# Kernel tuning notes

Measured on AMD Instinct MI355X. Metric: run time of the kernel, lower is better.

The kernel has to match this reference:

```python
import jax, jax.numpy as jnp
import numpy as np

NUM_HEADS = 16

def setup_inputs() -> dict:
    key = jax.random.key(0)
    ks = jax.random.split(key, 7)
    B, Q, K, D = 4, 512, 4096, 1024
    return {
        'query':  jax.random.normal(ks[0], (B, Q, D), dtype=jnp.float32),
        'memory': jax.random.normal(ks[1], (B, K, D), dtype=jnp.float32),
        'bias':   jax.random.normal(ks[2], (B, K), dtype=jnp.float32),
        'Wq': jax.random.normal(ks[3], (D, D), dtype=jnp.float32) * (D ** -0.5),
        'Wk': jax.random.normal(ks[4], (D, D), dtype=jnp.float32) * (D ** -0.5),
        'Wv': jax.random.normal(ks[5], (D, D), dtype=jnp.float32) * (D ** -0.5),
        'Wo': jax.random.normal(ks[6], (D, D), dtype=jnp.float32) * (D ** -0.5),
    }

def reference(query, memory, bias, Wq, Wk, Wv, Wo):
    B, Qn, _ = query.shape
    _, Kn, _ = memory.shape
    H = NUM_HEADS
    E = Wq.shape[1]
    dh = E // H
    scale = dh ** -0.5
    # projections (bias-free linears), split heads: [B, H, len, dh]
    q = (query @ Wq).reshape(B, Qn, H, dh).transpose(0, 2, 1, 3)
    k = (memory @ Wk).reshape(B, Kn, H, dh).transpose(0, 2, 1, 3)
    v = (memory @ Wv).reshape(B, Kn, H, dh).transpose(0, 2, 1, 3)
    scores = jnp.einsum('bhqd,bhkd->bhqk', q, k) * scale
    scores = scores + bias[:, None, None, :]          # additive support bias over K
    weights = jax.nn.softmax(scores, axis=-1)          # dropout p=0.0 -> identity
    out = jnp.einsum('bhqk,bhkd->bhqd', weights, v)
    out = out.transpose(0, 2, 1, 3).reshape(B, Qn, E)
    return out @ Wo
```

## Files before the change

### kernel.cpp

```cpp
#include <hip/hip_runtime.h>

typedef __attribute__((ext_vector_type(8))) short bf16x8;
typedef __attribute__((ext_vector_type(4))) short bf16x4;
typedef __attribute__((ext_vector_type(4))) float f32x4;

#define MFMA32(a,b,c) __builtin_amdgcn_mfma_f32_16x16x32_bf16((a),(b),(c),0,0,0)
#define MFMA16(a,b,c) __builtin_amdgcn_mfma_f32_16x16x16bf16_1k((a),(b),(c),0,0,0)
#define LOG2E 1.44269504f

__device__ __forceinline__ unsigned short f2bf(float f) {
  unsigned int u = __float_as_uint(f);
  u += 0x7fffu + ((u >> 16) & 1u);
  return (unsigned short)(u >> 16);
}

__device__ __forceinline__ void cp16(const void* g, void* l) {
  __builtin_amdgcn_global_load_lds((const __attribute__((address_space(1))) void*)g,
                                   (__attribute__((address_space(3))) void*)l, 16, 0, 0);
}

__global__ void conv_both(const float* __restrict__ q, const float* __restrict__ m,
                          const float* __restrict__ bias,
                          unsigned short* __restrict__ qo, unsigned short* __restrict__ mo,
                          float* __restrict__ bz) {
  int i = blockIdx.x * 256 + threadIdx.x;
  if (i < 524288) {
    float4 v = ((const float4*)q)[i];
    ushort4 o; o.x = f2bf(v.x); o.y = f2bf(v.y); o.z = f2bf(v.z); o.w = f2bf(v.w);
    ((ushort4*)qo)[i] = o;
  } else if (i < 4718592) {
    int j = i - 524288;
    float4 v = ((const float4*)m)[j];
    ushort4 o; o.x = f2bf(v.x); o.y = f2bf(v.y); o.z = f2bf(v.z); o.w = f2bf(v.w);
    ((ushort4*)mo)[j] = o;
  } else {
    int j = i - 4718592;
    float4 v = ((const float4*)bias)[j];
    float4 o;
    o.x = __builtin_fmaf(v.x, LOG2E, -16.f);
    o.y = __builtin_fmaf(v.y, LOG2E, -16.f);
    o.z = __builtin_fmaf(v.z, LOG2E, -16.f);
    o.w = __builtin_fmaf(v.w, LOG2E, -16.f);
    ((float4*)bz)[j] = o;
  }
}

__global__ void transpose4(const float* __restrict__ Wq, const float* __restrict__ Wk,
                           const float* __restrict__ Wv, const float* __restrict__ Wo,
                           unsigned short* __restrict__ dst) {
  __shared__ float t[32][33];
  int z = blockIdx.z;
  const float* W = (z == 0) ? Wq : (z == 1) ? Wk : (z == 2) ? Wv : Wo;
  unsigned short* WT = dst + (size_t)z * 1048576;
  int bx = blockIdx.x * 32, by = blockIdx.y * 32;
  int x = threadIdx.x, y0 = threadIdx.y;
#pragma unroll
  for (int r = 0; r < 4; ++r)
    t[y0 + r * 8][x] = W[(size_t)(by + y0 + r * 8) * 1024 + bx + x];
  __syncthreads();
#pragma unroll
  for (int r = 0; r < 4; ++r)
    WT[(size_t)(bx + y0 + r * 8) * 1024 + by + x] = f2bf(t[x][y0 + r * 8]);
}

__global__ __launch_bounds__(512, 2) void gemm_kv(
    const unsigned short* __restrict__ A,
    const unsigned short* __restrict__ Bk,
    const unsigned short* __restrict__ Bv,
    unsigned short* __restrict__ Kp,
    unsigned short* __restrict__ Vt)
{
  __shared__ __attribute__((aligned(16))) unsigned short lds[65536];
  const int tid = threadIdx.x;
  const int w = tid >> 6, lane = tid & 63;
  const int lh = lane & 15, q4 = lane >> 4;
  const int id = blockIdx.x;
  const int xcd = id & 7, j = id >> 3;
  const int tm = (xcd * 8 + (j >> 3)) * 256;
  const int tn = (j & 7) * 128;
  const int wm = (w >> 1) * 64, wn = (w & 1) * 64;

  const int r8 = lane >> 3;
  const int scol = ((lane & 7) ^ r8) * 8;
  const int srow = w * 8 + r8;
  const int fs0 = ((0 + q4) ^ (lh & 7)) * 8;
  const int fs1 = ((4 + q4) ^ (lh & 7)) * 8;

  const unsigned short* Ag = A  + (size_t)tm * 1024 + scol;
  const unsigned short* Kg = Bk + (size_t)tn * 1024 + scol;
  const unsigned short* Vg = Bv + (size_t)tn * 1024 + scol;

#define STG_A(BUF,KT,I) cp16(Ag + (size_t)((I)*64 + srow) * 1024 + (KT)*64, \
                             lds + (BUF)*32768 + (I)*4096 + w*512)
#define STG_K(BUF,KT,I) cp16(Kg + (size_t)((I)*64 + srow) * 1024 + (KT)*64, \
                             lds + (BUF)*32768 + 16384 + (I)*4096 + w*512)
#define STG_V(BUF,KT,I) cp16(Vg + (size_t)((I)*64 + srow) * 1024 + (KT)*64, \
                             lds + (BUF)*32768 + 24576 + (I)*4096 + w*512)

  f32x4 acck[4][4] = {}, accv[4][4] = {};

  STG_A(0, 0, 0); STG_A(0, 0, 1); STG_A(0, 0, 2); STG_A(0, 0, 3);
  STG_K(0, 0, 0); STG_K(0, 0, 1);
  STG_V(0, 0, 0); STG_V(0, 0, 1);

  for (int t = 0; t < 16; ++t) {
    const unsigned short* bse = lds + (t & 1) * 32768;
    const int nx = (t & 1) ^ 1;
    __syncthreads();
    if (t < 15) {
      STG_A(nx, t + 1, 0); STG_A(nx, t + 1, 1);
      STG_A(nx, t + 1, 2); STG_A(nx, t + 1, 3);
      STG_K(nx, t + 1, 0); STG_K(nx, t + 1, 1);
      STG_V(nx, t + 1, 0); STG_V(nx, t + 1, 1);
    }
    {
      bf16x8 a0[4], bk0[4], bv0[4];
#pragma unroll
      for (int m = 0; m < 4; ++m)
        a0[m] = *(const bf16x8*)(bse + (wm + m * 16 + lh) * 64 + fs0);
#pragma unroll
      for (int n = 0; n < 4; ++n) {
        bk0[n] = *(const bf16x8*)(bse + 16384 + (wn + n * 16 + lh) * 64 + fs0);
        bv0[n] = *(const bf16x8*)(bse + 24576 + (wn + n * 16 + lh) * 64 + fs0);
      }
      __builtin_amdgcn_s_setprio(1);
#pragma unroll
      for (int m = 0; m < 4; ++m)
#pragma unroll
        for (int n = 0; n < 4; ++n) {
          acck[m][n] = MFMA32(a0[m], bk0[n], acck[m][n]);
          accv[m][n] = MFMA32(a0[m], bv0[n], accv[m][n]);
        }
      __builtin_amdgcn_s_setprio(0);
    }
    {
      bf16x8 a1[4], bk1[4], bv1[4];
#pragma unroll
      for (int m = 0; m < 4; ++m)
        a1[m] = *(const bf16x8*)(bse + (wm + m * 16 + lh) * 64 + fs1);
#pragma unroll
      for (int n = 0; n < 4; ++n) {
        bk1[n] = *(const bf16x8*)(bse + 16384 + (wn + n * 16 + lh) * 64 + fs1);
        bv1[n] = *(const bf16x8*)(bse + 24576 + (wn + n * 16 + lh) * 64 + fs1);
      }
      __builtin_amdgcn_s_setprio(1);
#pragma unroll
      for (int m = 0; m < 4; ++m)
#pragma unroll
        for (int n = 0; n < 4; ++n) {
          acck[m][n] = MFMA32(a1[m], bk1[n], acck[m][n]);
          accv[m][n] = MFMA32(a1[m], bv1[n], accv[m][n]);
        }
      __builtin_amdgcn_s_setprio(0);
    }
  }

#undef STG_A
#undef STG_K
#undef STG_V

#pragma unroll
  for (int m = 0; m < 4; ++m)
#pragma unroll
    for (int n = 0; n < 4; ++n) {
      int row = tm + wm + m * 16 + q4 * 4;
      int col = tn + wn + n * 16 + lh;
#pragma unroll
      for (int e = 0; e < 4; ++e)
        Kp[(size_t)(row + e) * 1024 + col] = f2bf(acck[m][n][e]);
    }

  __syncthreads();
#pragma unroll
  for (int m = 0; m < 4; ++m)
#pragma unroll
    for (int n = 0; n < 4; ++n) {
      int row = wm + m * 16 + q4 * 4;
      int col = wn + n * 16 + lh;
      ushort4 v4;
      v4.x = f2bf(accv[m][n][0]); v4.y = f2bf(accv[m][n][1]);
      v4.z = f2bf(accv[m][n][2]); v4.w = f2bf(accv[m][n][3]);
      *(ushort4*)(lds + col * 256 + (row ^ ((col & 31) << 3))) = v4;
    }
  __syncthreads();
#pragma unroll
  for (int p = 0; p < 8; ++p) {
    int col = p * 16 + (tid >> 5);
    int jb = tid & 31;
    const unsigned short* src = lds + col * 256 + ((jb ^ (col & 31)) << 3);
    *(int4*)(Vt + (size_t)(tn + col) * 16384 + tm + jb * 8) = *(const int4*)src;
  }
}

__global__ __launch_bounds__(256) void gemm_bt64(
    const unsigned short* __restrict__ A, const unsigned short* __restrict__ B,
    float* __restrict__ Cf, unsigned short* __restrict__ Cb,
    int M, int N, int K, float scale)
{
  __shared__ __attribute__((aligned(16))) unsigned short lds[12288];
  int w = threadIdx.x >> 6, lane = threadIdx.x & 63;
  int lh = lane & 15, q4 = lane >> 4;
  int tm = blockIdx.y * 128, tn = blockIdx.x * 64;
  int wm = (w & 1) * 64, wn = (w >> 1) * 32;

  int srow = lane >> 2;
  int scol = ((lane & 3) ^ ((lane >> 3) & 3)) << 3;
  int q4s = (q4 ^ ((lh >> 1) & 3)) << 3;

#define STG64(BUF,K0)                                                          \
  {                                                                            \
    _Pragma("unroll") for (int i = 0; i < 2; ++i) {                            \
      int c = w * 2 + i;                                                       \
      cp16(A + (size_t)(tm + c * 16 + srow) * K + (K0) + scol,                 \
           lds + (BUF) * 6144 + c * 512);                                      \
    }                                                                          \
    cp16(B + (size_t)(tn + w * 16 + srow) * K + (K0) + scol,                   \
         lds + (BUF) * 6144 + 4096 + w * 512);                                 \
  }

  f32x4 acc[4][2] = {};
  const int nst = K >> 5;

  STG64(0, 0);

  for (int t = 0; t < nst; ++t) {
    const unsigned short* bse = lds + (t & 1) * 6144;
    __syncthreads();
    if (t + 1 < nst) STG64((t & 1) ^ 1, (t + 1) << 5);
    bf16x8 afr[4], bfr[2];
#pragma unroll
    for (int r = 0; r < 4; ++r)
      afr[r] = *(const bf16x8*)(bse + (wm + r * 16 + lh) * 32 + q4s);
#pragma unroll
    for (int c = 0; c < 2; ++c)
      bfr[c] = *(const bf16x8*)(bse + 4096 + (wn + c * 16 + lh) * 32 + q4s);
    __builtin_amdgcn_s_setprio(1);
#pragma unroll
    for (int r = 0; r < 4; ++r)
#pragma unroll
      for (int c = 0; c < 2; ++c)
        acc[r][c] = MFMA32(afr[r], bfr[c], acc[r][c]);
    __builtin_amdgcn_s_setprio(0);
  }
#undef STG64

#pragma unroll
  for (int r = 0; r < 4; ++r)
#pragma unroll
    for (int c = 0; c < 2; ++c)
#pragma unroll
      for (int e = 0; e < 4; ++e) {
        int row = tm + wm + r * 16 + q4 * 4 + e;
        int col = tn + wn + c * 16 + lh;
        if (Cb) Cb[(size_t)row * N + col] = f2bf(acc[r][c][e] * scale);
        else    Cf[(size_t)row * N + col] = acc[r][c][e] * scale;
      }
}

__global__ __launch_bounds__(256) void attn_kernel(
    const unsigned short* __restrict__ Q, const unsigned short* __restrict__ Kp,
    const unsigned short* __restrict__ VT, const float* __restrict__ bz,
    float* __restrict__ po, float* __restrict__ lp)
{
  __shared__ __attribute__((aligned(16))) unsigned short Klds[4096];
  __shared__ __attribute__((aligned(16))) unsigned short Vlds[4096];
  int w = threadIdx.x >> 6, lane = threadIdx.x & 63;
  int lh = lane & 15, q4 = lane >> 4;

  int id = blockIdx.x;
  int xcd = id & 7, j = id >> 3;
  int ql = j & 7;
  int half = ql & 1, qt = ql >> 1;
  int bh = (j >> 3) * 8 + xcd;
  int b = bh >> 4, h = bh & 15;
  int q0 = qt * 128;
  int t00 = half * 2048;

  const unsigned short* Qb = Q + (size_t)(b * 512 + q0 + w * 32) * 1024 + h * 64;
  const unsigned short* Kb = Kp + (size_t)(b * 4096) * 1024 + h * 64;
  const unsigned short* Vb = VT + (size_t)(h * 64) * 16384 + b * 4096;
  const float* bzg = bz + (size_t)b * 4096;

  bf16x8 bq[2][2];
#pragma unroll
  for (int s = 0; s < 2; ++s)
#pragma unroll
    for (int th = 0; th < 2; ++th)
      bq[s][th] = *(const bf16x8*)(Qb + (size_t)(s * 16 + lh) * 1024 + th * 32 + q4 * 8);

  f32x4 oa[2][4] = {};
  float ls[2] = {0.f, 0.f};

  int rl = lane >> 3, blk = lane & 7;
  int sw = ((blk ^ rl) * 8);

  for (int ti = 0; ti < 32; ++ti) {
    int t = t00 + ti * 64;
#pragma unroll
    for (int r = 0; r < 2; ++r) {
      int seg = r * 4 + w;
      int row = seg * 8 + rl;
      cp16(Kb + (size_t)(t + row) * 1024 + sw, Klds + seg * 512);
      cp16(Vb + (size_t)row * 16384 + t + sw, Vlds + seg * 512);
    }
    __syncthreads();

    float4 bz4[4];
#pragma unroll
    for (int c = 0; c < 4; ++c)
      bz4[c] = *(const float4*)(bzg + t + c * 16 + q4 * 4);

    bf16x8 kf[4][2];
#pragma unroll
    for (int c = 0; c < 4; ++c)
#pragma unroll
      for (int th = 0; th < 2; ++th)
        kf[c][th] = *(const bf16x8*)(Klds + (c * 16 + lh) * 64 + (((th << 2) + q4) ^ (lh & 7)) * 8);
    bf16x4 vf[4][4];
#pragma unroll
    for (int c = 0; c < 4; ++c)
#pragma unroll
      for (int c2 = 0; c2 < 4; ++c2)
        vf[c][c2] = *(const bf16x4*)(Vlds + (c2 * 16 + lh) * 64 +
                                     (((c << 1) + (q4 >> 1)) ^ (lh & 7)) * 8 + (q4 & 1) * 4);

#pragma unroll
    for (int s = 0; s < 2; ++s) {
#pragma unroll
      for (int c = 0; c < 4; ++c) {
        f32x4 z = {};
        z = MFMA32(kf[c][0], bq[s][0], z);
        z = MFMA32(kf[c][1], bq[s][1], z);
        float bzf[4] = {bz4[c].x, bz4[c].y, bz4[c].z, bz4[c].w};
        bf16x4 pb;
        float ps = 0.f;
#pragma unroll
        for (int e = 0; e < 4; ++e) {
          float p = __builtin_amdgcn_exp2f(z[e] + bzf[e]);
          ps += p;
          pb[e] = (short)f2bf(p);
        }
        ls[s] += ps;
#pragma unroll
        for (int c2 = 0; c2 < 4; ++c2)
          oa[s][c2] = MFMA16(vf[c][c2], pb, oa[s][c2]);
      }
    }
    __syncthreads();
  }

#pragma unroll
  for (int s = 0; s < 2; ++s) {
    ls[s] += __shfl_xor(ls[s], 16);
    ls[s] += __shfl_xor(ls[s], 32);
  }

  int sl = bh * 4 + qt;
  float* pslice = po + (size_t)(half * 256 + sl) * 8192;
#pragma unroll
  for (int s = 0; s < 2; ++s) {
    if (q4 == 0) lp[half * 32768 + sl * 128 + w * 32 + s * 16 + lh] = ls[s];
#pragma unroll
    for (int c2 = 0; c2 < 4; ++c2)
#pragma unroll
      for (int e = 0; e < 4; ++e)
        pslice[(c2 * 16 + q4 * 4 + e) * 128 + w * 32 + s * 16 + lh] = oa[s][c2][e];
  }
}

__global__ void norm_kernel(const float* __restrict__ po, const float* __restrict__ lp,
                            unsigned short* __restrict__ ao) {
  int g = blockIdx.x * 256 + threadIdx.x;
  int d8 = (g & 7) * 8;
  int rowid = g >> 3;
  int bh = rowid >> 9, rq = rowid & 511, qt = rq >> 7, qcol = rq & 127;
  int sl = bh * 4 + qt;
  const float* p0 = po + (size_t)sl * 8192;
  const float* p1 = po + (size_t)(256 + sl) * 8192;
  float l = lp[sl * 128 + qcol] + lp[32768 + sl * 128 + qcol];
  float inv = 1.f / l;
  unsigned short o8[8];
#pragma unroll
  for (int k = 0; k < 8; ++k)
    o8[k] = f2bf((p0[(d8 + k) * 128 + qcol] + p1[(d8 + k) * 128 + qcol]) * inv);
  int b = bh >> 4, h = bh & 15;
  unsigned short* dst = ao + (size_t)(b * 512 + qt * 128 + qcol) * 1024 + h * 64 + d8;
  *(ushort4*)dst = *(ushort4*)o8;
  *(ushort4*)(dst + 4) = *(ushort4*)(o8 + 4);
}

extern "C" void kernel_launch(void* const* d_in, const int* in_sizes, int n_in,
                              void* d_out, int out_size, void* d_ws, size_t ws_size,
                              hipStream_t stream) {
  const float* query  = (const float*)d_in[0];
  const float* memory = (const float*)d_in[1];
  const float* bias   = (const float*)d_in[2];
  const float* Wq     = (const float*)d_in[3];
  const float* Wk     = (const float*)d_in[4];
  const float* Wv     = (const float*)d_in[5];
  const float* Wo     = (const float*)d_in[6];
  float* out = (float*)d_out;

  unsigned short* ws  = (unsigned short*)d_ws;
  unsigned short* qbf = ws;
  unsigned short* mbf = qbf + 2097152;
  unsigned short* WqT = mbf + 16777216;
  unsigned short* WkT = WqT + 1048576;
  unsigned short* WvT = WkT + 1048576;
  unsigned short* WoT = WvT + 1048576;
  unsigned short* qp  = WoT + 1048576;
  unsigned short* kp  = qp + 2097152;
  unsigned short* vT  = kp + 16777216;
  unsigned short* ao  = vT + 16777216;
  float* bzw = (float*)(ao + 2097152);
  float* po = (float*)ws;
  float* lp = po + 4194304;

  conv_both<<<18448, 256, 0, stream>>>(query, memory, bias, qbf, mbf, bzw);
  transpose4<<<dim3(32, 32, 4), dim3(32, 8), 0, stream>>>(Wq, Wk, Wv, Wo, WqT);

  gemm_bt64<<<dim3(16, 16), 256, 0, stream>>>(qbf, WqT, nullptr, qp, 2048, 1024, 1024, 0.125f * LOG2E);
  gemm_kv<<<512, 512, 0, stream>>>(mbf, WkT, WvT, kp, vT);

  attn_kernel<<<512, 256, 0, stream>>>(qp, kp, vT, bzw, po, lp);
  norm_kernel<<<1024, 256, 0, stream>>>(po, lp, ao);

  gemm_bt64<<<dim3(16, 16), 256, 0, stream>>>(ao, WoT, out, nullptr, 2048, 1024, 1024, 1.f);
}
```

Baseline: 289.7 us.

## Load K/V weight fragments directly from global and deepen LDS staging

In the fused K/V projection kernel, the weight operands (Bk, Bv) are no longer staged through LDS. Each wave reads its MFMA fragments straight from global memory, which frees LDS for a 4-buffer ring of A tiles that are prefetched two k-steps at a time with one barrier per pair. The generic gemm_bt64 also moves to a 4-stage ring, issuing two stages per barrier, which halves the number of syncs. The risk is higher global/L2 traffic and exposed latency for the uncached direct B loads, since these wait on global memory instead of LDS.

```diff
diff --git a/kernel.cpp b/kernel.cpp
--- a/kernel.cpp
+++ b/kernel.cpp
@@ -86,78 +86,77 @@
   const int fs0 = ((0 + q4) ^ (lh & 7)) * 8;
   const int fs1 = ((4 + q4) ^ (lh & 7)) * 8;
 
-  const unsigned short* Ag = A  + (size_t)tm * 1024 + scol;
-  const unsigned short* Kg = Bk + (size_t)tn * 1024 + scol;
-  const unsigned short* Vg = Bv + (size_t)tn * 1024 + scol;
-
-#define STG_A(BUF,KT,I) cp16(Ag + (size_t)((I)*64 + srow) * 1024 + (KT)*64, \
-                             lds + (BUF)*32768 + (I)*4096 + w*512)
-#define STG_K(BUF,KT,I) cp16(Kg + (size_t)((I)*64 + srow) * 1024 + (KT)*64, \
-                             lds + (BUF)*32768 + 16384 + (I)*4096 + w*512)
-#define STG_V(BUF,KT,I) cp16(Vg + (size_t)((I)*64 + srow) * 1024 + (KT)*64, \
-                             lds + (BUF)*32768 + 24576 + (I)*4096 + w*512)
+  const unsigned short* Ag = A + (size_t)tm * 1024 + scol;
+  const unsigned short* Kg = Bk + (size_t)(tn + wn + lh) * 1024 + q4 * 8;
+  const unsigned short* Vg = Bv + (size_t)(tn + wn + lh) * 1024 + q4 * 8;
+
+#define STG_A(BUF,KT) do {                                                    \
+    cp16(Ag + (size_t)(  0 + srow) * 1024 + (KT)*64, lds + (BUF)*16384 +    w*512); \
+    cp16(Ag + (size_t)( 64 + srow) * 1024 + (KT)*64, lds + (BUF)*16384 + 4096 + w*512); \
+    cp16(Ag + (size_t)(128 + srow) * 1024 + (KT)*64, lds + (BUF)*16384 + 8192 + w*512); \
+    cp16(Ag + (size_t)(192 + srow) * 1024 + (KT)*64, lds + (BUF)*16384 + 12288 + w*512); \
+  } while (0)
 
   f32x4 acck[4][4] = {}, accv[4][4] = {};
 
-  STG_A(0, 0, 0); STG_A(0, 0, 1); STG_A(0, 0, 2); STG_A(0, 0, 3);
-  STG_K(0, 0, 0); STG_K(0, 0, 1);
-  STG_V(0, 0, 0); STG_V(0, 0, 1);
-
-  for (int t = 0; t < 16; ++t) {
-    const unsigned short* bse = lds + (t & 1) * 32768;
-    const int nx = (t & 1) ^ 1;
+  STG_A(0, 0);
+  STG_A(1, 1);
+
+  for (int s = 0; s < 8; ++s) {
     __syncthreads();
-    if (t < 15) {
-      STG_A(nx, t + 1, 0); STG_A(nx, t + 1, 1);
-      STG_A(nx, t + 1, 2); STG_A(nx, t + 1, 3);
-      STG_K(nx, t + 1, 0); STG_K(nx, t + 1, 1);
-      STG_V(nx, t + 1, 0); STG_V(nx, t + 1, 1);
-    }
-    {
-      bf16x8 a0[4], bk0[4], bv0[4];
-#pragma unroll
-      for (int m = 0; m < 4; ++m)
-        a0[m] = *(const bf16x8*)(bse + (wm + m * 16 + lh) * 64 + fs0);
-#pragma unroll
-      for (int n = 0; n < 4; ++n) {
-        bk0[n] = *(const bf16x8*)(bse + 16384 + (wn + n * 16 + lh) * 64 + fs0);
-        bv0[n] = *(const bf16x8*)(bse + 24576 + (wn + n * 16 + lh) * 64 + fs0);
+    if (s < 7) {
+      STG_A((2 * s + 2) & 3, 2 * s + 2);
+      STG_A((2 * s + 3) & 3, 2 * s + 3);
+    }
+#pragma unroll
+    for (int u = 0; u < 2; ++u) {
+      const int tt = 2 * s + u;
+      const unsigned short* bse = lds + (tt & 3) * 16384;
+      const int ko = tt * 64;
+      {
+        bf16x8 a0[4], bk0[4], bv0[4];
+#pragma unroll
+        for (int m = 0; m < 4; ++m)
+          a0[m] = *(const bf16x8*)(bse + (wm + m * 16 + lh) * 64 + fs0);
+#pragma unroll
+        for (int n = 0; n < 4; ++n) {
+          bk0[n] = *(const bf16x8*)(Kg + (size_t)(n * 16) * 1024 + ko);
+          bv0[n] = *(const bf16x8*)(Vg + (size_t)(n * 16) * 1024 + ko);
+        }
+        __builtin_amdgcn_s_setprio(1);
+#pragma unroll
+        for (int m = 0; m < 4; ++m)
+#pragma unroll
+          for (int n = 0; n < 4; ++n) {
+            acck[m][n] = MFMA32(a0[m], bk0[n], acck[m][n]);
+            accv[m][n] = MFMA32(a0[m], bv0[n], accv[m][n]);
+          }
+        __builtin_amdgcn_s_setprio(0);
       }
-      __builtin_amdgcn_s_setprio(1);
-#pragma unroll
-      for (int m = 0; m < 4; ++m)
+      {
+        bf16x8 a1[4], bk1[4], bv1[4];
+#pragma unroll
+        for (int m = 0; m < 4; ++m)
+          a1[m] = *(const bf16x8*)(bse + (wm + m * 16 + lh) * 64 + fs1);
 #pragma unroll
         for (int n = 0; n < 4; ++n) {
-          acck[m][n] = MFMA32(a0[m], bk0[n], acck[m][n]);
-          accv[m][n] = MFMA32(a0[m], bv0[n], accv[m][n]);
+          bk1[n] = *(const bf16x8*)(Kg + (size_t)(n * 16) * 1024 + ko + 32);
+          bv1[n] = *(const bf16x8*)(Vg + (size_t)(n * 16) * 1024 + ko + 32);
         }
-      __builtin_amdgcn_s_setprio(0);
-    }
-    {
-      bf16x8 a1[4], bk1[4], bv1[4];
-#pragma unroll
-      for (int m = 0; m < 4; ++m)
-        a1[m] = *(const bf16x8*)(bse + (wm + m * 16 + lh) * 64 + fs1);
-#pragma unroll
-      for (int n = 0; n < 4; ++n) {
-        bk1[n] = *(const bf16x8*)(bse + 16384 + (wn + n * 16 + lh) * 64 + fs1);
-        bv1[n] = *(const bf16x8*)(bse + 24576 + (wn + n * 16 + lh) * 64 + fs1);
+        __builtin_amdgcn_s_setprio(1);
+#pragma unroll
+        for (int m = 0; m < 4; ++m)
+#pragma unroll
+          for (int n = 0; n < 4; ++n) {
+            acck[m][n] = MFMA32(a1[m], bk1[n], acck[m][n]);
+            accv[m][n] = MFMA32(a1[m], bv1[n], accv[m][n]);
+          }
+        __builtin_amdgcn_s_setprio(0);
       }
-      __builtin_amdgcn_s_setprio(1);
-#pragma unroll
-      for (int m = 0; m < 4; ++m)
-#pragma unroll
-        for (int n = 0; n < 4; ++n) {
-          acck[m][n] = MFMA32(a1[m], bk1[n], acck[m][n]);
-          accv[m][n] = MFMA32(a1[m], bv1[n], accv[m][n]);
-        }
-      __builtin_amdgcn_s_setprio(0);
     }
   }
 
 #undef STG_A
-#undef STG_K
-#undef STG_V
 
 #pragma unroll
   for (int m = 0; m < 4; ++m)
@@ -197,7 +196,7 @@
     float* __restrict__ Cf, unsigned short* __restrict__ Cb,
     int M, int N, int K, float scale)
 {
-  __shared__ __attribute__((aligned(16))) unsigned short lds[12288];
+  __shared__ __attribute__((aligned(16))) unsigned short lds[24576];
   int w = threadIdx.x >> 6, lane = threadIdx.x & 63;
   int lh = lane & 15, q4 = lane >> 4;
   int tm = blockIdx.y * 128, tn = blockIdx.x * 64;
@@ -219,28 +218,35 @@
   }
 
   f32x4 acc[4][2] = {};
-  const int nst = K >> 5;
+  const int nw = K >> 6;
 
   STG64(0, 0);
-
-  for (int t = 0; t < nst; ++t) {
-    const unsigned short* bse = lds + (t & 1) * 6144;
+  STG64(1, 32);
+
+  for (int s = 0; s < nw; ++s) {
     __syncthreads();
-    if (t + 1 < nst) STG64((t & 1) ^ 1, (t + 1) << 5);
-    bf16x8 afr[4], bfr[2];
-#pragma unroll
-    for (int r = 0; r < 4; ++r)
-      afr[r] = *(const bf16x8*)(bse + (wm + r * 16 + lh) * 32 + q4s);
-#pragma unroll
-    for (int c = 0; c < 2; ++c)
-      bfr[c] = *(const bf16x8*)(bse + 4096 + (wn + c * 16 + lh) * 32 + q4s);
-    __builtin_amdgcn_s_setprio(1);
-#pragma unroll
-    for (int r = 0; r < 4; ++r)
+    if (s + 1 < nw) {
+      STG64((2 * s + 2) & 3, (2 * s + 2) << 5);
+      STG64((2 * s + 3) & 3, (2 * s + 3) << 5);
+    }
+#pragma unroll
+    for (int u = 0; u < 2; ++u) {
+      const unsigned short* bse = lds + ((2 * s + u) & 3) * 6144;
+      bf16x8 afr[4], bfr[2];
+#pragma unroll
+      for (int r = 0; r < 4; ++r)
+        afr[r] = *(const bf16x8*)(bse + (wm + r * 16 + lh) * 32 + q4s);
 #pragma unroll
       for (int c = 0; c < 2; ++c)
-        acc[r][c] = MFMA32(afr[r], bfr[c], acc[r][c]);
-    __builtin_amdgcn_s_setprio(0);
+        bfr[c] = *(const bf16x8*)(bse + 4096 + (wn + c * 16 + lh) * 32 + q4s);
+      __builtin_amdgcn_s_setprio(1);
+#pragma unroll
+      for (int r = 0; r < 4; ++r)
+#pragma unroll
+        for (int c = 0; c < 2; ++c)
+          acc[r][c] = MFMA32(afr[r], bfr[c], acc[r][c]);
+      __builtin_amdgcn_s_setprio(0);
+    }
   }
 #undef STG64
 
```

Result: slower. 363.2 us (+25.4%).
